# Kernel optimization log

Measured on AMD Instinct MI355X. Metric: run time of the kernel, lower is better.

Reference implementation:

```python
import jax, jax.numpy as jnp
import numpy as np


def setup_inputs() -> dict:
    key = jax.random.key(0)
    ks = jax.random.split(key, 6)
    B, L, D, H, W = 32, 1024, 128, 128, 9
    F = D + W  # feature dim after one-hot positional embed
    rn = lambda k, shape, s: (jax.random.normal(k, shape, jnp.float32) * s)
    return {
        "embeddings": rn(ks[0], (B, L, D), 1.0),
        "masks": jnp.ones((B, L), jnp.float32),  # unused in math (as in source)
        "w1_w": rn(ks[1], (F, H), 0.05),
        "w1_b": jnp.zeros((H,), jnp.float32),
        "w2_w": rn(ks[2], (F, H), 0.05),
        "w2_b": jnp.zeros((H,), jnp.float32),
        "v_w": rn(ks[3], (H, 1), 0.05),
        "v_b": jnp.zeros((1,), jnp.float32),
        "cnn_w": rn(ks[4], (F * W, H), 0.02),
        "cnn_b": jnp.zeros((H,), jnp.float32),
        "window_size": 9,
    }


def reference(embeddings, masks, w1_w, w1_b, w2_w, w2_b, v_w, v_b, cnn_w, cnn_b, window_size):
    # Vectorized form of the per-position loop in LocalConvolutionLayer.forward.
    B, L, D = embeddings.shape
    W = window_size
    half = W // 2
    # Zero-pad then gather all sliding windows at once: [B, L, W, D]
    padded = jnp.pad(embeddings, ((0, 0), (half, half), (0, 0)))
    idx = jnp.arange(L)[:, None] + jnp.arange(W)[None, :]  # [L, W]
    win = padded[:, idx, :]
    # One-hot within-window positional embedding, concatenated on channels -> F = D + W
    pos = jnp.broadcast_to(jnp.eye(W, dtype=embeddings.dtype), (B, L, W, W))
    ctx = jnp.concatenate([win, pos], axis=-1)  # [B, L, W, F]
    ent = ctx[:, :, half, :]                    # center token, [B, L, F]
    # AttentionLayer: v(tanh(w1(ent)[:,None] + w2(ctx)))
    re = ent @ w1_w + w1_b                      # [B, L, H]
    rc = ctx @ w2_w + w2_b                      # [B, L, W, H]
    scores = jnp.tanh(re[:, :, None, :] + rc) @ v_w + v_b  # [B, L, W, 1]
    weights = jax.nn.softmax(scores, axis=2)
    out = (weights * ctx).reshape(B, L, W * ctx.shape[-1])  # [B, L, W*F]
    return out @ cnn_w + cnn_b                  # [B, L, H]
```

## Files before the change

### kernel.cpp

```cpp
#include <hip/hip_runtime.h>
#include <hip/hip_bf16.h>


typedef __attribute__((ext_vector_type(8))) short bf16x8;
typedef __attribute__((ext_vector_type(4))) float f32x4;

#define LL 1024
#define TANHK 2.885390081777927f

__device__ __forceinline__ unsigned short f2bf(float f) {
  unsigned int u = __float_as_uint(f);
  u = u + 0x7FFFu + ((u >> 16) & 1u);
  return (unsigned short)(u >> 16);
}
__device__ __forceinline__ float bf2f(unsigned short us) {
  return __uint_as_float(((unsigned int)us) << 16);
}

__global__ __launch_bounds__(256) void prep_kernel(
    const float* __restrict__ w1, const float* __restrict__ w2,
    const float* __restrict__ cnn,
    unsigned short* __restrict__ W12Frag, unsigned short* __restrict__ CwFrag) {
  int gid = blockIdx.x * 256 + threadIdx.x;
  if (blockIdx.x < 128) {
    int d = gid >> 8, n = gid & 255;
    float v = (n < 128) ? w1[d * 128 + n] : w2[d * 128 + (n - 128)];
    int tile = (n >> 4) * 4 + (d >> 5);
    int lane = ((d >> 3) & 3) * 16 + (n & 15);
    W12Frag[(tile * 64 + lane) * 8 + (d & 7)] = f2bf(v);
  } else {
    int idx = gid - 32768;
    int h = idx & 127;
    int wd = idx >> 7;
    int w = wd >> 7, d = wd & 127;
    float v = cnn[(w * 137 + d) * 128 + h];
    int tile = (w * 8 + (h >> 4)) * 4 + (d >> 5);
    int lane = ((d >> 3) & 3) * 16 + (h & 15);
    CwFrag[(tile * 64 + lane) * 8 + (d & 7)] = f2bf(v);
  }
}

__global__ __launch_bounds__(512, 4) void mega_kernel(
    const float* __restrict__ emb,
    const unsigned short* __restrict__ W12Frag,
    const unsigned short* __restrict__ CwFrag,
    const float* __restrict__ w1, const float* __restrict__ w1b,
    const float* __restrict__ w2, const float* __restrict__ w2b,
    const float* __restrict__ vw,
    const float* __restrict__ cnn, const float* __restrict__ cnnb,
    float* __restrict__ out) {
  extern __shared__ __align__(16) unsigned char smem[];
  uint4* E            = (uint4*)smem;
  unsigned short* Hs  = (unsigned short*)(smem + 20480);
  float* pwL          = (float*)(smem + 61440);
  float* vwL          = (float*)(smem + 66048);
  float* wtT          = (float*)(smem + 66560);

  int tid = threadIdx.x;
  int bid = blockIdx.x;
  int b = bid >> 4, l0 = (bid & 15) << 6;
  int lane = tid & 63, wid = tid >> 6;
  int l15 = lane & 15, l4 = lane >> 4;
  const bf16x8* Wf = (const bf16x8*)W12Frag;
  const bf16x8* Cf = (const bf16x8*)CwFrag;

  #pragma unroll
  for (int s = 0; s < 5; ++s) {
    int i = tid + s * 512;
    if (i < 1280) {
      int er = i >> 4, g = i & 15;
      int t = l0 + er - 4;
      uint4 v = {0u, 0u, 0u, 0u};
      if (er < 72 && t >= 0 && t < LL) {
        const float4* src = (const float4*)(emb + ((size_t)(b * LL + t) << 7) + g * 8);
        float4 x0 = src[0], x1 = src[1];
        v.x = f2bf(x0.x) | ((unsigned)f2bf(x0.y) << 16);
        v.y = f2bf(x0.z) | ((unsigned)f2bf(x0.w) << 16);
        v.z = f2bf(x1.x) | ((unsigned)f2bf(x1.y) << 16);
        v.w = f2bf(x1.z) | ((unsigned)f2bf(x1.w) << 16);
      }
      E[er * 16 + (g ^ (er & 7))] = v;
    } else if (i < 2432) {
      int idx = i - 1280;
      int w = idx >> 7, h = idx & 127;
      pwL[idx] = TANHK * (w2[(128 + w) * 128 + h] + w2b[h] +
                          w1[132 * 128 + h] + w1b[h]);
    } else {
      int h = i - 2432;
      vwL[h] = vw[h];
    }
  }
  __syncthreads();

  const bf16x8* Eb = (const bf16x8*)E;
  #pragma unroll
  for (int it = 0; it < 2; ++it) {
    int job = it == 0 ? wid : 8;
    if (it == 0 || wid == 0) {
      int part = job >= 4;
      int er0 = part ? (job - 4) * 16 : 4 + job * 16;
      f32x4 acc[8];
      #pragma unroll
      for (int nn = 0; nn < 8; ++nn) acc[nn] = (f32x4){0.f, 0.f, 0.f, 0.f};
      #pragma unroll
      for (int kk = 0; kk < 4; ++kk) {
        int gk = kk * 4 + l4;
        int er = er0 + l15;
        bf16x8 aF = Eb[er * 16 + (gk ^ (er & 7))];
        #pragma unroll
        for (int nn = 0; nn < 8; ++nn) {
          bf16x8 bF = Wf[((part * 8 + nn) * 4 + kk) * 64 + lane];
          acc[nn] = __builtin_amdgcn_mfma_f32_16x16x32_bf16(aF, bF, acc[nn], 0, 0, 0);
        }
      }
      unsigned short* Hp = Hs + part * 10240;
      int hxor = (((er0 >> 2) + l4) & 3) << 4;
      #pragma unroll
      for (int nn = 0; nn < 8; ++nn)
        #pragma unroll
        for (int j = 0; j < 4; ++j) {
          int i2 = er0 + l4 * 4 + j;
          Hp[i2 * 128 + ((nn * 16 + l15) ^ hxor)] = f2bf(TANHK * acc[nn][j]);
        }
    }
  }
  __syncthreads();

  {
    int q = lane >> 4, u = lane & 15, u8 = u * 8;
    const unsigned short* Hs1 = Hs;
    const unsigned short* Hs2 = Hs + 10240;
    #pragma unroll
    for (int pass = 0; pass < 2; ++pass) {
      int r = wid * 8 + pass * 4 + q;
      int fi = r + 4;
      int fxor = ((fi >> 2) & 3) << 4;
      bf16x8 fraw = *(const bf16x8*)&Hs1[fi * 128 + (u8 ^ fxor)];
      float fr[8];
      #pragma unroll
      for (int j = 0; j < 8; ++j) fr[j] = bf2f((unsigned short)fraw[j]);
      f32x4 vr0 = *(const f32x4*)&vwL[u8];
      f32x4 vr1 = *(const f32x4*)&vwL[u8 + 4];
      float sc[9];
      #pragma unroll
      for (int w = 0; w < 9; ++w) {
        int gi = r + w;
        int gxor = ((gi >> 2) & 3) << 4;
        bf16x8 graw = *(const bf16x8*)&Hs2[gi * 128 + (u8 ^ gxor)];
        f32x4 pw0 = *(const f32x4*)&pwL[w * 128 + u8];
        f32x4 pw1 = *(const f32x4*)&pwL[w * 128 + u8 + 4];
        float a = 0.f;
        #pragma unroll
        for (int j = 0; j < 4; ++j) {
          float e = exp2f(fr[j] + bf2f((unsigned short)graw[j]) + pw0[j]);
          a = fmaf(vr0[j], __builtin_amdgcn_rcpf(1.f + e), a);
        }
        #pragma unroll
        for (int j = 0; j < 4; ++j) {
          float e = exp2f(fr[4 + j] + bf2f((unsigned short)graw[4 + j]) + pw1[j]);
          a = fmaf(vr1[j], __builtin_amdgcn_rcpf(1.f + e), a);
        }
        a += __shfl_xor(a, 1, 64);
        a += __shfl_xor(a, 2, 64);
        a += __shfl_xor(a, 4, 64);
        a += __shfl_xor(a, 8, 64);
        sc[w] = a;
      }
      float mn = sc[0];
      #pragma unroll
      for (int w = 1; w < 9; ++w) mn = fminf(mn, sc[w]);
      float p[9], sum = 0.f;
      #pragma unroll
      for (int w = 0; w < 9; ++w) { p[w] = exp2f(TANHK * (mn - sc[w])); sum += p[w]; }
      float inv = __builtin_amdgcn_rcpf(sum);
      if (u < 9) {
        float wv = p[0];
        #pragma unroll
        for (int w = 1; w < 9; ++w) wv = (u == w) ? p[w] : wv;
        wtT[u * 68 + r] = wv * inv;
      }
    }
  }
  __syncthreads();

  int wr = wid >> 2, wc = wid & 3;
  int h0 = wc * 32 + l15;
  f32x4 fin[2][2];
  #pragma unroll
  for (int m = 0; m < 2; ++m)
    #pragma unroll
    for (int n = 0; n < 2; ++n) fin[m][n] = (f32x4){0.f, 0.f, 0.f, 0.f};
  #pragma unroll
  for (int w = 0; w < 9; ++w) {
    f32x4 tmp[2][2];
    #pragma unroll
    for (int m = 0; m < 2; ++m)
      #pragma unroll
      for (int n = 0; n < 2; ++n) tmp[m][n] = (f32x4){0.f, 0.f, 0.f, 0.f};
    #pragma unroll
    for (int kk = 0; kk < 4; ++kk) {
      int gk = kk * 4 + l4;
      bf16x8 aF[2];
      #pragma unroll
      for (int m = 0; m < 2; ++m) {
        int er = wr * 32 + m * 16 + l15 + w;
        aF[m] = Eb[er * 16 + (gk ^ (er & 7))];
      }
      #pragma unroll
      for (int n = 0; n < 2; ++n) {
        bf16x8 bF = Cf[((w * 8 + wc * 2 + n) * 4 + kk) * 64 + lane];
        #pragma unroll
        for (int m = 0; m < 2; ++m)
          tmp[m][n] = __builtin_amdgcn_mfma_f32_16x16x32_bf16(aF[m], bF, tmp[m][n], 0, 0, 0);
      }
    }
    float cp0 = cnn[(w * 138 + 128) * 128 + h0];
    float cp1 = cnn[(w * 138 + 128) * 128 + h0 + 16];
    #pragma unroll
    for (int m = 0; m < 2; ++m) {
      f32x4 wt4 = *(const f32x4*)&wtT[w * 68 + wr * 32 + m * 16 + l4 * 4];
      #pragma unroll
      for (int j = 0; j < 4; ++j) {
        fin[m][0][j] += wt4[j] * (tmp[m][0][j] + cp0);
        fin[m][1][j] += wt4[j] * (tmp[m][1][j] + cp1);
      }
    }
  }
  float cb0 = cnnb[h0], cb1 = cnnb[h0 + 16];
  #pragma unroll
  for (int m = 0; m < 2; ++m)
    #pragma unroll
    for (int j = 0; j < 4; ++j) {
      int r = wr * 32 + m * 16 + l4 * 4 + j;
      size_t o = ((size_t)(b * LL + l0 + r) << 7) + h0;
      out[o]      = fin[m][0][j] + cb0;
      out[o + 16] = fin[m][1][j] + cb1;
    }
}

extern "C" void kernel_launch(void* const* d_in, const int* in_sizes, int n_in,
                              void* d_out, int out_size, void* d_ws, size_t ws_size,
                              hipStream_t stream) {
  const float* emb  = (const float*)d_in[0];
  const float* w1   = (const float*)d_in[2];
  const float* w1b  = (const float*)d_in[3];
  const float* w2   = (const float*)d_in[4];
  const float* w2b  = (const float*)d_in[5];
  const float* vw   = (const float*)d_in[6];
  const float* cnn  = (const float*)d_in[8];
  const float* cnnb = (const float*)d_in[9];
  float* out = (float*)d_out;

  char* ws = (char*)d_ws;
  unsigned short* W12Frag = (unsigned short*)(ws);
  unsigned short* CwFrag  = (unsigned short*)(ws + 65536);

  prep_kernel<<<704, 256, 0, stream>>>(w1, w2, cnn, W12Frag, CwFrag);
  mega_kernel<<<512, 512, 69008, stream>>>(emb, W12Frag, CwFrag, w1, w1b, w2, w2b,
                                           vw, cnn, cnnb, out);
}
```

Measured before the change: 130.8 us.

## Halve block tile to 32 rows and keep center projections in registers

Each block now covers 32 sequence positions with 256 threads instead of 64 positions with 512 threads, and the grid doubles to 1024 blocks. The ent projection (w1 path) is no longer written to shared memory as a bf16 tile. It stays in MFMA accumulator registers and is read directly in the score loop. The w2 context tile is stored unswizzled with padding using packed v_cvt_pk_bf16 conversions, which shrinks LDS so more blocks can fit per CU. The trade-off is a larger halo overhead (8 of every 40 rows are redundant) and each wave now recomputes the ent projection.

```diff
diff --git a/kernel.cpp b/kernel.cpp
--- a/kernel.cpp
+++ b/kernel.cpp
@@ -15,6 +15,11 @@
 }
 __device__ __forceinline__ float bf2f(unsigned short us) {
   return __uint_as_float(((unsigned int)us) << 16);
+}
+__device__ __forceinline__ unsigned cvt_pk_bf16(float lo, float hi) {
+  unsigned r;
+  asm("v_cvt_pk_bf16_f32 %0, %1, %2" : "=v"(r) : "v"(lo), "v"(hi));
+  return r;
 }
 
 __global__ __launch_bounds__(256) void prep_kernel(
@@ -40,7 +45,7 @@
   }
 }
 
-__global__ __launch_bounds__(512, 4) void mega_kernel(
+__global__ __launch_bounds__(256, 5) void mega_kernel(
     const float* __restrict__ emb,
     const unsigned short* __restrict__ W12Frag,
     const unsigned short* __restrict__ CwFrag,
@@ -50,141 +55,154 @@
     const float* __restrict__ cnn, const float* __restrict__ cnnb,
     float* __restrict__ out) {
   extern __shared__ __align__(16) unsigned char smem[];
-  uint4* E            = (uint4*)smem;
-  unsigned short* Hs  = (unsigned short*)(smem + 20480);
-  float* pwL          = (float*)(smem + 61440);
-  float* vwL          = (float*)(smem + 66048);
-  float* wtT          = (float*)(smem + 66560);
+  uint4* E           = (uint4*)smem;
+  unsigned short* GP = (unsigned short*)(smem + 12288);
+  float* pwP         = (float*)(smem + 25344);
+  float* vwP         = (float*)(smem + 29952);
+  float* wtT         = (float*)(smem + 30464);
 
   int tid = threadIdx.x;
   int bid = blockIdx.x;
-  int b = bid >> 4, l0 = (bid & 15) << 6;
+  int b = bid >> 5, l0 = (bid & 31) << 5;
   int lane = tid & 63, wid = tid >> 6;
   int l15 = lane & 15, l4 = lane >> 4;
   const bf16x8* Wf = (const bf16x8*)W12Frag;
   const bf16x8* Cf = (const bf16x8*)CwFrag;
 
   #pragma unroll
+  for (int s = 0; s < 3; ++s) {
+    int i = tid + s * 256;
+    int er = i >> 4, g = i & 15;
+    int t = l0 + er - 4;
+    uint4 v = {0u, 0u, 0u, 0u};
+    if (er < 40 && t >= 0 && t < LL) {
+      const float4* src = (const float4*)(emb + ((size_t)(b * LL + t) << 7) + g * 8);
+      float4 x0 = src[0], x1 = src[1];
+      v.x = cvt_pk_bf16(x0.x, x0.y);
+      v.y = cvt_pk_bf16(x0.z, x0.w);
+      v.z = cvt_pk_bf16(x1.x, x1.y);
+      v.w = cvt_pk_bf16(x1.z, x1.w);
+    }
+    E[er * 16 + (g ^ (er & 7))] = v;
+  }
+  #pragma unroll
   for (int s = 0; s < 5; ++s) {
-    int i = tid + s * 512;
-    if (i < 1280) {
-      int er = i >> 4, g = i & 15;
-      int t = l0 + er - 4;
-      uint4 v = {0u, 0u, 0u, 0u};
-      if (er < 72 && t >= 0 && t < LL) {
-        const float4* src = (const float4*)(emb + ((size_t)(b * LL + t) << 7) + g * 8);
-        float4 x0 = src[0], x1 = src[1];
-        v.x = f2bf(x0.x) | ((unsigned)f2bf(x0.y) << 16);
-        v.y = f2bf(x0.z) | ((unsigned)f2bf(x0.w) << 16);
-        v.z = f2bf(x1.x) | ((unsigned)f2bf(x1.y) << 16);
-        v.w = f2bf(x1.z) | ((unsigned)f2bf(x1.w) << 16);
-      }
-      E[er * 16 + (g ^ (er & 7))] = v;
-    } else if (i < 2432) {
-      int idx = i - 1280;
-      int w = idx >> 7, h = idx & 127;
-      pwL[idx] = TANHK * (w2[(128 + w) * 128 + h] + w2b[h] +
-                          w1[132 * 128 + h] + w1b[h]);
+    int i = tid + s * 256;
+    if (i < 1152) {
+      int w = i >> 7, p = i & 127;
+      int h = ((p & 7) << 4) + (p >> 3);
+      pwP[i] = TANHK * (w2[(128 + w) * 128 + h] + w2b[h] +
+                        w1[132 * 128 + h] + w1b[h]);
     } else {
-      int h = i - 2432;
-      vwL[h] = vw[h];
+      int p = i - 1152;
+      int h = ((p & 7) << 4) + (p >> 3);
+      vwP[p] = vw[h];
     }
   }
   __syncthreads();
 
   const bf16x8* Eb = (const bf16x8*)E;
-  #pragma unroll
-  for (int it = 0; it < 2; ++it) {
-    int job = it == 0 ? wid : 8;
-    if (it == 0 || wid == 0) {
-      int part = job >= 4;
-      int er0 = part ? (job - 4) * 16 : 4 + job * 16;
-      f32x4 acc[8];
-      #pragma unroll
-      for (int nn = 0; nn < 8; ++nn) acc[nn] = (f32x4){0.f, 0.f, 0.f, 0.f};
-      #pragma unroll
-      for (int kk = 0; kk < 4; ++kk) {
-        int gk = kk * 4 + l4;
-        int er = er0 + l15;
-        bf16x8 aF = Eb[er * 16 + (gk ^ (er & 7))];
-        #pragma unroll
-        for (int nn = 0; nn < 8; ++nn) {
-          bf16x8 bF = Wf[((part * 8 + nn) * 4 + kk) * 64 + lane];
-          acc[nn] = __builtin_amdgcn_mfma_f32_16x16x32_bf16(aF, bF, acc[nn], 0, 0, 0);
-        }
-      }
-      unsigned short* Hp = Hs + part * 10240;
-      int hxor = (((er0 >> 2) + l4) & 3) << 4;
-      #pragma unroll
-      for (int nn = 0; nn < 8; ++nn)
-        #pragma unroll
-        for (int j = 0; j < 4; ++j) {
-          int i2 = er0 + l4 * 4 + j;
-          Hp[i2 * 128 + ((nn * 16 + l15) ^ hxor)] = f2bf(TANHK * acc[nn][j]);
-        }
+  f32x4 af[8];
+  #pragma unroll
+  for (int nn = 0; nn < 8; ++nn) af[nn] = (f32x4){0.f, 0.f, 0.f, 0.f};
+  {
+    int er0f = 4 + ((wid & 1) << 4);
+    #pragma unroll
+    for (int kk = 0; kk < 4; ++kk) {
+      int gk = kk * 4 + l4;
+      int er = er0f + l15;
+      bf16x8 aF = Eb[er * 16 + (gk ^ (er & 7))];
+      #pragma unroll
+      for (int nn = 0; nn < 8; ++nn) {
+        bf16x8 bF = Wf[(nn * 4 + kk) * 64 + lane];
+        af[nn] = __builtin_amdgcn_mfma_f32_16x16x32_bf16(aF, bF, af[nn], 0, 0, 0);
+      }
+    }
+  }
+  if (wid < 3) {
+    int er0g = wid << 4;
+    f32x4 ag[8];
+    #pragma unroll
+    for (int nn = 0; nn < 8; ++nn) ag[nn] = (f32x4){0.f, 0.f, 0.f, 0.f};
+    #pragma unroll
+    for (int kk = 0; kk < 4; ++kk) {
+      int gk = kk * 4 + l4;
+      int er = er0g + l15;
+      bf16x8 aF = Eb[er * 16 + (gk ^ (er & 7))];
+      #pragma unroll
+      for (int nn = 0; nn < 8; ++nn) {
+        bf16x8 bF = Wf[((8 + nn) * 4 + kk) * 64 + lane];
+        ag[nn] = __builtin_amdgcn_mfma_f32_16x16x32_bf16(aF, bF, ag[nn], 0, 0, 0);
+      }
+    }
+    #pragma unroll
+    for (int j = 0; j < 4; ++j) {
+      int row = er0g + l4 * 4 + j;
+      uint4 v;
+      v.x = cvt_pk_bf16(TANHK * ag[0][j], TANHK * ag[1][j]);
+      v.y = cvt_pk_bf16(TANHK * ag[2][j], TANHK * ag[3][j]);
+      v.z = cvt_pk_bf16(TANHK * ag[4][j], TANHK * ag[5][j]);
+      v.w = cvt_pk_bf16(TANHK * ag[6][j], TANHK * ag[7][j]);
+      *(uint4*)(GP + row * 136 + l15 * 8) = v;
     }
   }
   __syncthreads();
 
   {
-    int q = lane >> 4, u = lane & 15, u8 = u * 8;
-    const unsigned short* Hs1 = Hs;
-    const unsigned short* Hs2 = Hs + 10240;
-    #pragma unroll
-    for (int pass = 0; pass < 2; ++pass) {
-      int r = wid * 8 + pass * 4 + q;
-      int fi = r + 4;
-      int fxor = ((fi >> 2) & 3) << 4;
-      bf16x8 fraw = *(const bf16x8*)&Hs1[fi * 128 + (u8 ^ fxor)];
-      float fr[8];
-      #pragma unroll
-      for (int j = 0; j < 8; ++j) fr[j] = bf2f((unsigned short)fraw[j]);
-      f32x4 vr0 = *(const f32x4*)&vwL[u8];
-      f32x4 vr1 = *(const f32x4*)&vwL[u8 + 4];
-      float sc[9];
-      #pragma unroll
-      for (int w = 0; w < 9; ++w) {
-        int gi = r + w;
-        int gxor = ((gi >> 2) & 3) << 4;
-        bf16x8 graw = *(const bf16x8*)&Hs2[gi * 128 + (u8 ^ gxor)];
-        f32x4 pw0 = *(const f32x4*)&pwL[w * 128 + u8];
-        f32x4 pw1 = *(const f32x4*)&pwL[w * 128 + u8 + 4];
-        float a = 0.f;
-        #pragma unroll
-        for (int j = 0; j < 4; ++j) {
-          float e = exp2f(fr[j] + bf2f((unsigned short)graw[j]) + pw0[j]);
-          a = fmaf(vr0[j], __builtin_amdgcn_rcpf(1.f + e), a);
-        }
-        #pragma unroll
-        for (int j = 0; j < 4; ++j) {
-          float e = exp2f(fr[4 + j] + bf2f((unsigned short)graw[4 + j]) + pw1[j]);
-          a = fmaf(vr1[j], __builtin_amdgcn_rcpf(1.f + e), a);
-        }
-        a += __shfl_xor(a, 1, 64);
-        a += __shfl_xor(a, 2, 64);
-        a += __shfl_xor(a, 4, 64);
-        a += __shfl_xor(a, 8, 64);
-        sc[w] = a;
-      }
-      float mn = sc[0];
-      #pragma unroll
-      for (int w = 1; w < 9; ++w) mn = fminf(mn, sc[w]);
-      float p[9], sum = 0.f;
-      #pragma unroll
-      for (int w = 0; w < 9; ++w) { p[w] = exp2f(TANHK * (mn - sc[w])); sum += p[w]; }
-      float inv = __builtin_amdgcn_rcpf(sum);
-      if (u < 9) {
-        float wv = p[0];
-        #pragma unroll
-        for (int w = 1; w < 9; ++w) wv = (u == w) ? p[w] : wv;
-        wtT[u * 68 + r] = wv * inv;
-      }
-    }
+    int rbase = (wid & 1) << 4;
+    f32x4 vr0 = *(const f32x4*)(vwP + l15 * 8);
+    f32x4 vr1 = *(const f32x4*)(vwP + l15 * 8 + 4);
+
+#define DO_SCORE(J)                                                            \
+    {                                                                          \
+      int rl = rbase + l4 * 4 + (J);                                           \
+      float sc[9];                                                             \
+      _Pragma("unroll")                                                        \
+      for (int w = 0; w < 9; ++w) {                                            \
+        bf16x8 graw = *(const bf16x8*)(GP + (rl + w) * 136 + l15 * 8);         \
+        f32x4 pw0 = *(const f32x4*)(pwP + w * 128 + l15 * 8);                  \
+        f32x4 pw1 = *(const f32x4*)(pwP + w * 128 + l15 * 8 + 4);              \
+        float a = 0.f;                                                         \
+        _Pragma("unroll")                                                      \
+        for (int c = 0; c < 4; ++c) {                                          \
+          float e = exp2f(fmaf(af[c][(J)], TANHK,                              \
+                               bf2f((unsigned short)graw[c]) + pw0[c]));       \
+          a = fmaf(vr0[c], __builtin_amdgcn_rcpf(1.f + e), a);                 \
+        }                                                                      \
+        _Pragma("unroll")                                                      \
+        for (int c = 0; c < 4; ++c) {                                          \
+          float e = exp2f(fmaf(af[4 + c][(J)], TANHK,                          \
+                               bf2f((unsigned short)graw[4 + c]) + pw1[c]));   \
+          a = fmaf(vr1[c], __builtin_amdgcn_rcpf(1.f + e), a);                 \
+        }                                                                      \
+        a += __shfl_xor(a, 1, 64);                                             \
+        a += __shfl_xor(a, 2, 64);                                             \
+        a += __shfl_xor(a, 4, 64);                                             \
+        a += __shfl_xor(a, 8, 64);                                             \
+        sc[w] = a;                                                             \
+      }                                                                        \
+      float mn = sc[0];                                                        \
+      _Pragma("unroll")                                                        \
+      for (int w = 1; w < 9; ++w) mn = fminf(mn, sc[w]);                       \
+      float pp[9], sum = 0.f;                                                  \
+      _Pragma("unroll")                                                        \
+      for (int w = 0; w < 9; ++w) { pp[w] = exp2f(TANHK * (mn - sc[w])); sum += pp[w]; } \
+      float inv = __builtin_amdgcn_rcpf(sum);                                  \
+      if (l15 < 9) {                                                           \
+        float wv = pp[0];                                                      \
+        _Pragma("unroll")                                                      \
+        for (int w = 1; w < 9; ++w) wv = (l15 == w) ? pp[w] : wv;              \
+        wtT[l15 * 36 + rl] = wv * inv;                                         \
+      }                                                                        \
+    }
+
+    if (!(wid & 2)) { DO_SCORE(0); DO_SCORE(1); }
+    else            { DO_SCORE(2); DO_SCORE(3); }
+#undef DO_SCORE
   }
   __syncthreads();
 
-  int wr = wid >> 2, wc = wid & 3;
-  int h0 = wc * 32 + l15;
+  int h0 = (wid << 5) + l15;
   f32x4 fin[2][2];
   #pragma unroll
   for (int m = 0; m < 2; ++m)
@@ -203,12 +221,12 @@
       bf16x8 aF[2];
       #pragma unroll
       for (int m = 0; m < 2; ++m) {
-        int er = wr * 32 + m * 16 + l15 + w;
+        int er = m * 16 + l15 + w;
         aF[m] = Eb[er * 16 + (gk ^ (er & 7))];
       }
       #pragma unroll
       for (int n = 0; n < 2; ++n) {
-        bf16x8 bF = Cf[((w * 8 + wc * 2 + n) * 4 + kk) * 64 + lane];
+        bf16x8 bF = Cf[((w * 8 + (wid << 1) + n) * 4 + kk) * 64 + lane];
         #pragma unroll
         for (int m = 0; m < 2; ++m)
           tmp[m][n] = __builtin_amdgcn_mfma_f32_16x16x32_bf16(aF[m], bF, tmp[m][n], 0, 0, 0);
@@ -218,7 +236,7 @@
     float cp1 = cnn[(w * 138 + 128) * 128 + h0 + 16];
     #pragma unroll
     for (int m = 0; m < 2; ++m) {
-      f32x4 wt4 = *(const f32x4*)&wtT[w * 68 + wr * 32 + m * 16 + l4 * 4];
+      f32x4 wt4 = *(const f32x4*)(wtT + w * 36 + m * 16 + l4 * 4);
       #pragma unroll
       for (int j = 0; j < 4; ++j) {
         fin[m][0][j] += wt4[j] * (tmp[m][0][j] + cp0);
@@ -231,7 +249,7 @@
   for (int m = 0; m < 2; ++m)
     #pragma unroll
     for (int j = 0; j < 4; ++j) {
-      int r = wr * 32 + m * 16 + l4 * 4 + j;
+      int r = m * 16 + l4 * 4 + j;
       size_t o = ((size_t)(b * LL + l0 + r) << 7) + h0;
       out[o]      = fin[m][0][j] + cb0;
       out[o + 16] = fin[m][1][j] + cb1;
@@ -256,6 +274,6 @@
   unsigned short* CwFrag  = (unsigned short*)(ws + 65536);
 
   prep_kernel<<<704, 256, 0, stream>>>(w1, w2, cnn, W12Frag, CwFrag);
-  mega_kernel<<<512, 512, 69008, stream>>>(emb, W12Frag, CwFrag, w1, w1b, w2, w2b,
-                                           vw, cnn, cnnb, out);
-}
+  mega_kernel<<<1024, 256, 31760, stream>>>(emb, W12Frag, CwFrag, w1, w1b, w2, w2b,
+                                            vw, cnn, cnnb, out);
+}
```

Measured after the change: 141.0 us. 1.08x slower.
